# Kernel optimization log

Hardware: AMD Instinct MI355X
Metric: run time of the kernel (lower is better)

The kernel has to match this reference:

```python
import math
import jax, jax.numpy as jnp
import numpy as np

B, T, C, H = 2, 2048, 1024, 16

def setup_inputs() -> dict:
    key = jax.random.key(0)
    k1, k2, k3 = jax.random.split(key, 3)
    x = jax.random.normal(k1, (B, T, C), dtype=jnp.float32)
    W_kqv = jax.random.normal(k2, (C, 3 * C), dtype=jnp.float32) * (1.0 / math.sqrt(C))
    W_proj = jax.random.normal(k3, (C, C), dtype=jnp.float32) * (1.0 / math.sqrt(C))
    b_proj = jnp.zeros((C,), dtype=jnp.float32)
    return {"x": x, "W_kqv": W_kqv, "W_proj": W_proj, "b_proj": b_proj}

def reference(x, W_kqv, W_proj, b_proj):
    Bx, Tx, Cx = x.shape
    hs = Cx // H  # head size
    q, k, v = jnp.split(x @ W_kqv, 3, axis=2)  # each (B,T,C)
    # (B,T,C) -> (B,H,T,hs)
    q = q.reshape(Bx, Tx, H, hs).transpose(0, 2, 1, 3)
    k = k.reshape(Bx, Tx, H, hs).transpose(0, 2, 1, 3)
    v = v.reshape(Bx, Tx, H, hs).transpose(0, 2, 1, 3)
    attn = jnp.einsum('bhqd,bhkd->bhqk', q, k) / math.sqrt(hs)  # (B,H,T,T)
    causal = jnp.tril(jnp.ones((Tx, Tx), dtype=bool))
    attn = jnp.where(causal, attn, -jnp.inf)
    attn = jax.nn.softmax(attn, axis=-1)
    y = jnp.einsum('bhqk,bhkd->bhqd', attn, v)  # (B,H,T,hs)
    y = y.transpose(0, 2, 1, 3).reshape(Bx, Tx, Cx)
    return y @ W_proj + b_proj
```

## Files before the change

### kernel.cpp

```cpp
#include <hip/hip_runtime.h>


typedef unsigned short u16;
typedef unsigned int u32;
typedef __bf16 bf16x8 __attribute__((ext_vector_type(8)));
typedef float f32x4 __attribute__((ext_vector_type(4)));
typedef u32 u32x4 __attribute__((ext_vector_type(4)));
typedef u32 u32x2 __attribute__((ext_vector_type(2)));
typedef u16 u16x4 __attribute__((ext_vector_type(4)));

__device__ __forceinline__ u16 f2bf(float f) {
  u32 u = __float_as_uint(f);
  u32 r = u + 0x7FFFu + ((u >> 16) & 1u);
  return (u16)(r >> 16);
}

__device__ __forceinline__ u32 cvt_pk_bf16(float a, float b) {
  u32 r;
  asm("v_cvt_pk_bf16_f32 %0, %1, %2" : "=v"(r) : "v"(a), "v"(b));
  return r;
}

__device__ __forceinline__ bf16x8 ld_bf8(const u16* p) {
  union { u32x4 u; bf16x8 b; } x;
  x.u = *(const u32x4*)p;
  return x.b;
}

__device__ __forceinline__ void gld_lds16(const u16* g, u16* l) {
  __builtin_amdgcn_global_load_lds(
      (const __attribute__((address_space(1))) u32*)g,
      (__attribute__((address_space(3))) u32*)l, 16, 0, 0);
}

__device__ __forceinline__ void convT_body(const float* __restrict__ src,
                                           u16* __restrict__ dst, int R, int Cc,
                                           int r0, int c0, float* ls ) {
  int t = threadIdx.x;
  for (int u = t; u < 1024; u += 256) {
    int r = u >> 4, cs = (u & 15) << 2;
    float4 v = *(const float4*)&src[(size_t)(r0 + r) * Cc + (c0 + cs)];
    ls[r * 65 + cs] = v.x; ls[r * 65 + cs + 1] = v.y;
    ls[r * 65 + cs + 2] = v.z; ls[r * 65 + cs + 3] = v.w;
  }
  __syncthreads();
  for (int u = t; u < 1024; u += 256) {
    int n = u >> 4, ks = (u & 15) << 2;
    u16x4 o;
    o.x = f2bf(ls[ks * 65 + n]); o.y = f2bf(ls[(ks + 1) * 65 + n]);
    o.z = f2bf(ls[(ks + 2) * 65 + n]); o.w = f2bf(ls[(ks + 3) * 65 + n]);
    *(u16x4*)&dst[(size_t)(c0 + n) * R + (r0 + ks)] = o;
  }
}

__global__ __launch_bounds__(256) void prep_kernel(
    const float* __restrict__ x, const float* __restrict__ Wkqv,
    const float* __restrict__ Wproj, u16* __restrict__ xb,
    u16* __restrict__ wkqvT, u16* __restrict__ wprojT) {
  __shared__ float ls[64 * 65];
  int bx = blockIdx.x;
  if (bx < 2048) {
    int idx = bx * 256 + threadIdx.x;
    const float4* s4 = (const float4*)x;
    float4 a = s4[2 * idx], b = s4[2 * idx + 1];
    union { u16 h[8]; u32x4 v; } pk;
    pk.h[0] = f2bf(a.x); pk.h[1] = f2bf(a.y); pk.h[2] = f2bf(a.z); pk.h[3] = f2bf(a.w);
    pk.h[4] = f2bf(b.x); pk.h[5] = f2bf(b.y); pk.h[6] = f2bf(b.z); pk.h[7] = f2bf(b.w);
    *(u32x4*)&xb[(size_t)idx * 8] = pk.v;
  } else if (bx < 2816) {
    int idx = bx - 2048;
    convT_body(Wkqv, wkqvT, 1024, 3072, (idx & 15) * 64, (idx >> 4) * 64, ls);
  } else {
    int idx = bx - 2816;
    convT_body(Wproj, wprojT, 1024, 1024, (idx & 15) * 64, (idx >> 4) * 64, ls);
  }
}

__global__ __launch_bounds__(256) void qkv_gemm_kernel(
    const u16* __restrict__ A, const u16* __restrict__ Bt,
    u16* __restrict__ Qh, u16* __restrict__ Kh, u16* __restrict__ Vh, float qscale) {
  constexpr int K = 1024;
  __shared__ __align__(16) u16 As[128 * 32];
  __shared__ __align__(16) u16 Bs[128 * 32];
  int t = threadIdx.x;
  int wave = t >> 6, lane = t & 63, quad = lane >> 4, l16 = lane & 15;
  int wm = (wave >> 1) << 6, wn = (wave & 1) << 6;
  int m0 = blockIdx.x * 128, n0 = blockIdx.y * 128;
  f32x4 acc[4][4] = {};
  int u0 = t, u1 = t + 256;
  int ra0 = u0 >> 2, ca0 = ((u0 & 3) ^ ((u0 >> 3) & 3)) << 3;
  int ra1 = u1 >> 2, ca1 = ((u1 & 3) ^ ((u1 >> 3) & 3)) << 3;
  int swq = (quad ^ ((l16 >> 1) & 3)) << 3;
  for (int k0 = 0; k0 < K; k0 += 32) {
    gld_lds16(&A[(size_t)(m0 + ra0) * K + k0 + ca0], &As[u0 * 8]);
    gld_lds16(&A[(size_t)(m0 + ra1) * K + k0 + ca1], &As[u1 * 8]);
    gld_lds16(&Bt[(size_t)(n0 + ra0) * K + k0 + ca0], &Bs[u0 * 8]);
    gld_lds16(&Bt[(size_t)(n0 + ra1) * K + k0 + ca1], &Bs[u1 * 8]);
    __syncthreads();
    bf16x8 af[4], bfr[4];
    for (int r = 0; r < 4; ++r) af[r] = ld_bf8(&As[(wm + r * 16 + l16) * 32 + swq]);
    for (int c = 0; c < 4; ++c) bfr[c] = ld_bf8(&Bs[(wn + c * 16 + l16) * 32 + swq]);
    for (int r = 0; r < 4; ++r)
      for (int c = 0; c < 4; ++c)
        acc[r][c] = __builtin_amdgcn_mfma_f32_16x16x32_bf16(af[r], bfr[c], acc[r][c], 0, 0, 0);
    __syncthreads();
  }
  for (int r = 0; r < 4; ++r) {
    int rowbase = m0 + wm + r * 16 + quad * 4;
    for (int c = 0; c < 4; ++c) {
      int col = n0 + wn + c * 16 + l16;
      int seg = col >> 10;
      int cc = col & 1023;
      int h = cc >> 6, d = cc & 63;
      for (int i = 0; i < 4; ++i) {
        int row = rowbase + i;
        int b = row >> 11, tt = row & 2047;
        size_t off = (((size_t)(b * 16 + h)) * 2048 + tt) * 64 + d;
        float v = acc[r][c][i];
        if (seg == 0)      Qh[off] = f2bf(v * qscale);
        else if (seg == 1) Kh[off] = f2bf(v);
        else               Vh[off] = f2bf(v);
      }
    }
  }
}

__global__ __launch_bounds__(256) void vT_kernel(const u16* __restrict__ Vh,
                                                 u16* __restrict__ Vt) {
  __shared__ __align__(16) u16 ls[64 * 72];
  int t = threadIdx.x;
  int t0 = blockIdx.x * 64, bh = blockIdx.y;
  const u16* in = Vh + ((size_t)bh * 2048 + t0) * 64;
  for (int u = t; u < 512; u += 256) {
    int row = u >> 3, col = (u & 7) << 3;
    *(u32x4*)&ls[row * 72 + col] = *(const u32x4*)&in[(size_t)row * 64 + col];
  }
  __syncthreads();
  for (int u = t; u < 512; u += 256) {
    int d = u >> 3, tc = (u & 7) << 3;
    union { u16 h[8]; u32x4 v; } pk;
    for (int j = 0; j < 8; ++j) pk.h[j] = ls[(tc + j) * 72 + d];
    *(u32x4*)&Vt[((size_t)bh * 64 + d) * 2048 + t0 + tc] = pk.v;
  }
}

__global__ __launch_bounds__(256) void proj_gemm_kernel(
    const u16* __restrict__ A, const u16* __restrict__ Bt,
    float* __restrict__ out, const float* __restrict__ bias) {
  constexpr int K = 1024;
  __shared__ __align__(16) u16 As[64 * 32];
  __shared__ __align__(16) u16 Bs[64 * 32];
  int t = threadIdx.x;
  int wave = t >> 6, lane = t & 63, quad = lane >> 4, l16 = lane & 15;
  int wm = (wave >> 1) << 5, wn = (wave & 1) << 5;
  int m0 = blockIdx.x * 64, n0 = blockIdx.y * 64;
  f32x4 acc[2][2] = {};
  int u0 = t;
  int ra0 = u0 >> 2, ca0 = ((u0 & 3) ^ ((u0 >> 3) & 3)) << 3;
  int swq = (quad ^ ((l16 >> 1) & 3)) << 3;
  for (int k0 = 0; k0 < K; k0 += 32) {
    gld_lds16(&A[(size_t)(m0 + ra0) * K + k0 + ca0], &As[u0 * 8]);
    gld_lds16(&Bt[(size_t)(n0 + ra0) * K + k0 + ca0], &Bs[u0 * 8]);
    __syncthreads();
    bf16x8 af[2], bfr[2];
    for (int r = 0; r < 2; ++r) af[r] = ld_bf8(&As[(wm + r * 16 + l16) * 32 + swq]);
    for (int c = 0; c < 2; ++c) bfr[c] = ld_bf8(&Bs[(wn + c * 16 + l16) * 32 + swq]);
    for (int r = 0; r < 2; ++r)
      for (int c = 0; c < 2; ++c)
        acc[r][c] = __builtin_amdgcn_mfma_f32_16x16x32_bf16(af[r], bfr[c], acc[r][c], 0, 0, 0);
    __syncthreads();
  }
  for (int r = 0; r < 2; ++r) {
    int rowbase = m0 + wm + r * 16 + quad * 4;
    for (int c = 0; c < 2; ++c) {
      int col = n0 + wn + c * 16 + l16;
      float bv = bias[col];
      for (int i = 0; i < 4; ++i)
        out[(size_t)(rowbase + i) * 1024 + col] = acc[r][c][i] + bv;
    }
  }
}

__global__ __launch_bounds__(256, 4) void flash_kernel(
    const u16* __restrict__ Qh, const u16* __restrict__ Kh, const u16* __restrict__ Vt,
    u16* __restrict__ yb, float* __restrict__ Opart) {
  __shared__ __align__(16) u16 Ks[2][64 * 64];
  __shared__ __align__(16) u16 Vs[2][64 * 64];
  int t = threadIdx.x, wave = t >> 6, lane = t & 63, quad = lane >> 4, l16 = lane & 15;
  const unsigned char JT[22] = {9, 8, 7, 47, 63, 46, 62, 6, 45, 61, 44, 60,
                                5, 43, 59, 42, 58, 4, 3, 2, 1, 0};
  int id = blockIdx.x;
  int g = id / 176, r = id % 176;
  int bh = g * 8 + (r & 7);
  int jx = r >> 3;
  int code = JT[jx];
  int qtile = code & 15;
  int half = (code >> 4) & 1;
  bool partial = (code >> 5) != 0;
  int nkv = 2 * qtile + 2, mid = qtile + 1;
  int kvs = (partial && half) ? mid : 0;
  int kve = partial ? (half ? nkv : mid) : nkv;
  int sidx = 15 - qtile;
  int q0 = qtile << 7;
  const u16* Qb = Qh + (size_t)bh * 2048 * 64;
  const u16* Kb = Kh + (size_t)bh * 2048 * 64;
  const u16* Vb = Vt + (size_t)bh * 64 * 2048;
  int qlo = q0 + wave * 32;
  int qhi = qlo + 31;
  bf16x8 qa0, qa1, qa2, qa3;
  {
    int qr0 = qlo + l16;
    qa0 = ld_bf8(&Qb[(size_t)qr0 * 64 + quad * 8]);
    qa1 = ld_bf8(&Qb[(size_t)qr0 * 64 + 32 + quad * 8]);
    int qr1 = qr0 + 16;
    qa2 = ld_bf8(&Qb[(size_t)qr1 * 64 + quad * 8]);
    qa3 = ld_bf8(&Qb[(size_t)qr1 * 64 + 32 + quad * 8]);
  }
  f32x4 oacc0[4] = {}, oacc1[4] = {};
  float lsum0 = 0.f, lsum1 = 0.f;
  int u0 = wave * 128 + lane, u1 = u0 + 64;
  int r0 = u0 >> 3, p0 = u0 & 7, cb0 = (p0 - r0) & 7;
  int r1s = u1 >> 3, p1 = u1 & 7, cb1 = (p1 - r1s) & 7;
  int vsub = (quad & 1) * 4;
  int vc0 = quad >> 1;
  {
    int kv0 = kvs << 6;
    gld_lds16(&Kb[(size_t)(kv0 + r0) * 64 + cb0 * 8], &Ks[0][u0 * 8]);
    gld_lds16(&Kb[(size_t)(kv0 + r1s) * 64 + cb1 * 8], &Ks[0][u1 * 8]);
    gld_lds16(&Vb[(size_t)r0 * 2048 + kv0 + cb0 * 8], &Vs[0][u0 * 8]);
    gld_lds16(&Vb[(size_t)r1s * 2048 + kv0 + cb1 * 8], &Vs[0][u1 * 8]);
  }
  for (int j = kvs; j < kve; ++j) {
    int p = (j - kvs) & 1;
    asm volatile("s_waitcnt vmcnt(0)" ::: "memory");
    __builtin_amdgcn_s_barrier();
    asm volatile("" ::: "memory");
    if (j + 1 < kve) {
      int kn0 = (j + 1) << 6;
      int pn = p ^ 1;
      gld_lds16(&Kb[(size_t)(kn0 + r0) * 64 + cb0 * 8], &Ks[pn][u0 * 8]);
      gld_lds16(&Kb[(size_t)(kn0 + r1s) * 64 + cb1 * 8], &Ks[pn][u1 * 8]);
      gld_lds16(&Vb[(size_t)r0 * 2048 + kn0 + cb0 * 8], &Vs[pn][u0 * 8]);
      gld_lds16(&Vb[(size_t)r1s * 2048 + kn0 + cb1 * 8], &Vs[pn][u1 * 8]);
    }
    int kv0 = j << 6;
    if (kv0 > qhi) continue;
    const u16* Ksp = Ks[p];
    const u16* Vsp = Vs[p];
    bool maskit = (kv0 + 63 > qlo);
    u32 w0[4][2], w1[4][2];
    for (int c = 0; c < 4; ++c) {
      int krow = c * 16 + l16;
      bf16x8 kb0 = ld_bf8(&Ksp[krow * 64 + ((quad + krow) & 7) * 8]);
      bf16x8 kb1 = ld_bf8(&Ksp[krow * 64 + ((quad + 4 + krow) & 7) * 8]);
      f32x4 z0 = {0.f, 0.f, 0.f, 0.f}, z1 = {0.f, 0.f, 0.f, 0.f};
      z0 = __builtin_amdgcn_mfma_f32_16x16x32_bf16(kb0, qa0, z0, 0, 0, 0);
      z0 = __builtin_amdgcn_mfma_f32_16x16x32_bf16(kb1, qa1, z0, 0, 0, 0);
      z1 = __builtin_amdgcn_mfma_f32_16x16x32_bf16(kb0, qa2, z1, 0, 0, 0);
      z1 = __builtin_amdgcn_mfma_f32_16x16x32_bf16(kb1, qa3, z1, 0, 0, 0);
      float pe0[4], pe1[4];
      if (maskit) {
        int qg0 = qlo + l16, qg1 = qg0 + 16;
        for (int i = 0; i < 4; ++i) {
          int kv = kv0 + c * 16 + quad * 4 + i;
          float a = __builtin_amdgcn_exp2f(z0[i]);
          float b = __builtin_amdgcn_exp2f(z1[i]);
          if (kv > qg0) a = 0.f;
          if (kv > qg1) b = 0.f;
          lsum0 += a; lsum1 += b;
          pe0[i] = a; pe1[i] = b;
        }
      } else {
        for (int i = 0; i < 4; ++i) {
          float a = __builtin_amdgcn_exp2f(z0[i]);
          float b = __builtin_amdgcn_exp2f(z1[i]);
          lsum0 += a; lsum1 += b;
          pe0[i] = a; pe1[i] = b;
        }
      }
      w0[c][0] = cvt_pk_bf16(pe0[0], pe0[1]); w0[c][1] = cvt_pk_bf16(pe0[2], pe0[3]);
      w1[c][0] = cvt_pk_bf16(pe1[0], pe1[1]); w1[c][1] = cvt_pk_bf16(pe1[2], pe1[3]);
    }
    union { u32 uu[4]; bf16x8 b; } pf00, pf01, pf10, pf11;
    pf00.uu[0] = w0[0][0]; pf00.uu[1] = w0[0][1]; pf00.uu[2] = w0[1][0]; pf00.uu[3] = w0[1][1];
    pf01.uu[0] = w0[2][0]; pf01.uu[1] = w0[2][1]; pf01.uu[2] = w0[3][0]; pf01.uu[3] = w0[3][1];
    pf10.uu[0] = w1[0][0]; pf10.uu[1] = w1[0][1]; pf10.uu[2] = w1[1][0]; pf10.uu[3] = w1[1][1];
    pf11.uu[0] = w1[2][0]; pf11.uu[1] = w1[2][1]; pf11.uu[2] = w1[3][0]; pf11.uu[3] = w1[3][1];
    for (int dt = 0; dt < 4; ++dt) {
      int vrow = dt * 16 + l16;
      int rbase = vrow * 64 + vsub;
      union { u32x2 lo2; struct { u32 a, b; }; } h0lo, h0hi, h1lo, h1hi;
      h0lo.lo2 = *(const u32x2*)&Vsp[rbase + (((vc0)     + vrow) & 7) * 8];
      h0hi.lo2 = *(const u32x2*)&Vsp[rbase + (((vc0 + 2) + vrow) & 7) * 8];
      h1lo.lo2 = *(const u32x2*)&Vsp[rbase + (((vc0 + 4) + vrow) & 7) * 8];
      h1hi.lo2 = *(const u32x2*)&Vsp[rbase + (((vc0 + 6) + vrow) & 7) * 8];
      union { u32 uu[4]; bf16x8 b; } va0, va1;
      va0.uu[0] = h0lo.a; va0.uu[1] = h0lo.b; va0.uu[2] = h0hi.a; va0.uu[3] = h0hi.b;
      va1.uu[0] = h1lo.a; va1.uu[1] = h1lo.b; va1.uu[2] = h1hi.a; va1.uu[3] = h1hi.b;
      oacc0[dt] = __builtin_amdgcn_mfma_f32_16x16x32_bf16(va0.b, pf00.b, oacc0[dt], 0, 0, 0);
      oacc0[dt] = __builtin_amdgcn_mfma_f32_16x16x32_bf16(va1.b, pf01.b, oacc0[dt], 0, 0, 0);
      oacc1[dt] = __builtin_amdgcn_mfma_f32_16x16x32_bf16(va0.b, pf10.b, oacc1[dt], 0, 0, 0);
      oacc1[dt] = __builtin_amdgcn_mfma_f32_16x16x32_bf16(va1.b, pf11.b, oacc1[dt], 0, 0, 0);
    }
  }
  lsum0 += __shfl_xor(lsum0, 16);
  lsum0 += __shfl_xor(lsum0, 32);
  lsum1 += __shfl_xor(lsum1, 16);
  lsum1 += __shfl_xor(lsum1, 32);
  if (partial) {
    float* Op = Opart + ((size_t)(bh * 6 + sidx) * 2 + half) * 8320;
    int ql = wave * 32 + l16;
    for (int dt = 0; dt < 4; ++dt)
      *(f32x4*)&Op[ql * 64 + dt * 16 + quad * 4] = oacc0[dt];
    for (int dt = 0; dt < 4; ++dt)
      *(f32x4*)&Op[(ql + 16) * 64 + dt * 16 + quad * 4] = oacc1[dt];
    if (quad == 0) { Op[8192 + ql] = lsum0; Op[8192 + ql + 16] = lsum1; }
  } else {
    int b = bh >> 4, hd = bh & 15;
    float inv0 = 1.0f / lsum0, inv1 = 1.0f / lsum1;
    int qq0 = qlo + l16;
    size_t ro0 = ((size_t)(b * 2048 + qq0)) * 1024 + hd * 64;
    size_t ro1 = ro0 + (size_t)16 * 1024;
    for (int dt = 0; dt < 4; ++dt) {
      u32x2 pr;
      pr.x = cvt_pk_bf16(oacc0[dt][0] * inv0, oacc0[dt][1] * inv0);
      pr.y = cvt_pk_bf16(oacc0[dt][2] * inv0, oacc0[dt][3] * inv0);
      *(u32x2*)&yb[ro0 + dt * 16 + quad * 4] = pr;
      pr.x = cvt_pk_bf16(oacc1[dt][0] * inv1, oacc1[dt][1] * inv1);
      pr.y = cvt_pk_bf16(oacc1[dt][2] * inv1, oacc1[dt][3] * inv1);
      *(u32x2*)&yb[ro1 + dt * 16 + quad * 4] = pr;
    }
  }
}

__global__ __launch_bounds__(256) void combine_kernel(const float* __restrict__ Opart,
                                                      u16* __restrict__ yb) {
  int sidx = blockIdx.x, bh = blockIdx.y, t = threadIdx.x;
  int qtile = 15 - sidx;
  const float* A = Opart + (size_t)(bh * 6 + sidx) * 2 * 8320;
  const float* Bp = A + 8320;
  int q = t >> 1, d0 = (t & 1) << 5;
  float inv = 1.0f / (A[8192 + q] + Bp[8192 + q]);
  int b = bh >> 4, h = bh & 15;
  size_t off = ((size_t)(b * 2048 + (qtile << 7) + q)) * 1024 + h * 64 + d0;
  union { u16 hh[32]; u32x4 v[4]; } pk;
  for (int k = 0; k < 32; ++k)
    pk.hh[k] = f2bf((A[q * 64 + d0 + k] + Bp[q * 64 + d0 + k]) * inv);
  for (int s = 0; s < 4; ++s)
    *(u32x4*)&yb[off + s * 8] = pk.v[s];
}

extern "C" void kernel_launch(void* const* d_in, const int* in_sizes, int n_in,
                              void* d_out, int out_size, void* d_ws, size_t ws_size,
                              hipStream_t stream) {
  const float* x     = (const float*)d_in[0];
  const float* Wkqv  = (const float*)d_in[1];
  const float* Wproj = (const float*)d_in[2];
  const float* bproj = (const float*)d_in[3];
  float* out = (float*)d_out;

  u16* ws     = (u16*)d_ws;
  u16* xb     = ws;
  u16* wkqvT  = xb + (size_t)4096 * 1024;
  u16* wprojT = wkqvT + (size_t)3072 * 1024;
  u16* Qh     = wprojT + (size_t)1024 * 1024;
  u16* Kh     = Qh + (size_t)32 * 2048 * 64;
  u16* Vt     = Kh + (size_t)32 * 2048 * 64;
  u16* yb     = Vt + (size_t)32 * 2048 * 64;
  u16* Vh     = yb;
  float* Opart = (float*)ws;

  const float QSCALE = 0.18033688011112042f;

  prep_kernel<<<3072, 256, 0, stream>>>(x, Wkqv, Wproj, xb, wkqvT, wprojT);
  qkv_gemm_kernel<<<dim3(32, 24), 256, 0, stream>>>(xb, wkqvT, Qh, Kh, Vh, QSCALE);
  vT_kernel<<<dim3(32, 32), 256, 0, stream>>>(Vh, Vt);
  flash_kernel<<<704, 256, 0, stream>>>(Qh, Kh, Vt, yb, Opart);
  combine_kernel<<<dim3(6, 32), 256, 0, stream>>>(Opart, yb);
  proj_gemm_kernel<<<dim3(64, 16), 256, 0, stream>>>(yb, wprojT, out, bproj);
}
```

Baseline: 181.1 us.

## Double-buffer GEMM LDS tiles and fuse V transpose into QKV epilogue

Both GEMM kernels now use two LDS buffers, prefetching the next K-slice while MFMAs consume the current one, with one barrier per iteration instead of two. The QKV GEMM epilogue writes V directly in transposed layout (4 contiguous bf16 per store), which removes the separate vT kernel launch and its extra read/write pass. This doubles LDS use per block and relies on the manual vmcnt/barrier sequence being correct for the async LDS loads.

```diff
diff --git a/kernel.cpp b/kernel.cpp
--- a/kernel.cpp
+++ b/kernel.cpp
@@ -78,10 +78,10 @@
 
 __global__ __launch_bounds__(256) void qkv_gemm_kernel(
     const u16* __restrict__ A, const u16* __restrict__ Bt,
-    u16* __restrict__ Qh, u16* __restrict__ Kh, u16* __restrict__ Vh, float qscale) {
+    u16* __restrict__ Qh, u16* __restrict__ Kh, u16* __restrict__ Vt, float qscale) {
   constexpr int K = 1024;
-  __shared__ __align__(16) u16 As[128 * 32];
-  __shared__ __align__(16) u16 Bs[128 * 32];
+  __shared__ __align__(16) u16 As[2][128 * 32];
+  __shared__ __align__(16) u16 Bs[2][128 * 32];
   int t = threadIdx.x;
   int wave = t >> 6, lane = t & 63, quad = lane >> 4, l16 = lane & 15;
   int wm = (wave >> 1) << 6, wn = (wave & 1) << 6;
@@ -91,56 +91,50 @@
   int ra0 = u0 >> 2, ca0 = ((u0 & 3) ^ ((u0 >> 3) & 3)) << 3;
   int ra1 = u1 >> 2, ca1 = ((u1 & 3) ^ ((u1 >> 3) & 3)) << 3;
   int swq = (quad ^ ((l16 >> 1) & 3)) << 3;
+  gld_lds16(&A[(size_t)(m0 + ra0) * K + ca0], &As[0][u0 * 8]);
+  gld_lds16(&A[(size_t)(m0 + ra1) * K + ca1], &As[0][u1 * 8]);
+  gld_lds16(&Bt[(size_t)(n0 + ra0) * K + ca0], &Bs[0][u0 * 8]);
+  gld_lds16(&Bt[(size_t)(n0 + ra1) * K + ca1], &Bs[0][u1 * 8]);
   for (int k0 = 0; k0 < K; k0 += 32) {
-    gld_lds16(&A[(size_t)(m0 + ra0) * K + k0 + ca0], &As[u0 * 8]);
-    gld_lds16(&A[(size_t)(m0 + ra1) * K + k0 + ca1], &As[u1 * 8]);
-    gld_lds16(&Bt[(size_t)(n0 + ra0) * K + k0 + ca0], &Bs[u0 * 8]);
-    gld_lds16(&Bt[(size_t)(n0 + ra1) * K + k0 + ca1], &Bs[u1 * 8]);
-    __syncthreads();
+    int p = (k0 >> 5) & 1;
+    asm volatile("s_waitcnt vmcnt(0)" ::: "memory");
+    __builtin_amdgcn_s_barrier();
+    asm volatile("" ::: "memory");
+    if (k0 + 32 < K) {
+      int kn = k0 + 32, pn = p ^ 1;
+      gld_lds16(&A[(size_t)(m0 + ra0) * K + kn + ca0], &As[pn][u0 * 8]);
+      gld_lds16(&A[(size_t)(m0 + ra1) * K + kn + ca1], &As[pn][u1 * 8]);
+      gld_lds16(&Bt[(size_t)(n0 + ra0) * K + kn + ca0], &Bs[pn][u0 * 8]);
+      gld_lds16(&Bt[(size_t)(n0 + ra1) * K + kn + ca1], &Bs[pn][u1 * 8]);
+    }
     bf16x8 af[4], bfr[4];
-    for (int r = 0; r < 4; ++r) af[r] = ld_bf8(&As[(wm + r * 16 + l16) * 32 + swq]);
-    for (int c = 0; c < 4; ++c) bfr[c] = ld_bf8(&Bs[(wn + c * 16 + l16) * 32 + swq]);
+    for (int r = 0; r < 4; ++r) af[r] = ld_bf8(&As[p][(wm + r * 16 + l16) * 32 + swq]);
+    for (int c = 0; c < 4; ++c) bfr[c] = ld_bf8(&Bs[p][(wn + c * 16 + l16) * 32 + swq]);
     for (int r = 0; r < 4; ++r)
       for (int c = 0; c < 4; ++c)
         acc[r][c] = __builtin_amdgcn_mfma_f32_16x16x32_bf16(af[r], bfr[c], acc[r][c], 0, 0, 0);
-    __syncthreads();
   }
   for (int r = 0; r < 4; ++r) {
     int rowbase = m0 + wm + r * 16 + quad * 4;
+    int b = rowbase >> 11, tt = rowbase & 2047;
     for (int c = 0; c < 4; ++c) {
       int col = n0 + wn + c * 16 + l16;
       int seg = col >> 10;
       int cc = col & 1023;
       int h = cc >> 6, d = cc & 63;
-      for (int i = 0; i < 4; ++i) {
-        int row = rowbase + i;
-        int b = row >> 11, tt = row & 2047;
+      if (seg == 2) {
+        union { u16 hh[4]; u16x4 v; } o;
+        for (int i = 0; i < 4; ++i) o.hh[i] = f2bf(acc[r][c][i]);
+        *(u16x4*)&Vt[((size_t)(b * 16 + h) * 64 + d) * 2048 + tt] = o.v;
+      } else {
         size_t off = (((size_t)(b * 16 + h)) * 2048 + tt) * 64 + d;
-        float v = acc[r][c][i];
-        if (seg == 0)      Qh[off] = f2bf(v * qscale);
-        else if (seg == 1) Kh[off] = f2bf(v);
-        else               Vh[off] = f2bf(v);
+        if (seg == 0) {
+          for (int i = 0; i < 4; ++i) Qh[off + (size_t)i * 64] = f2bf(acc[r][c][i] * qscale);
+        } else {
+          for (int i = 0; i < 4; ++i) Kh[off + (size_t)i * 64] = f2bf(acc[r][c][i]);
+        }
       }
     }
-  }
-}
-
-__global__ __launch_bounds__(256) void vT_kernel(const u16* __restrict__ Vh,
-                                                 u16* __restrict__ Vt) {
-  __shared__ __align__(16) u16 ls[64 * 72];
-  int t = threadIdx.x;
-  int t0 = blockIdx.x * 64, bh = blockIdx.y;
-  const u16* in = Vh + ((size_t)bh * 2048 + t0) * 64;
-  for (int u = t; u < 512; u += 256) {
-    int row = u >> 3, col = (u & 7) << 3;
-    *(u32x4*)&ls[row * 72 + col] = *(const u32x4*)&in[(size_t)row * 64 + col];
-  }
-  __syncthreads();
-  for (int u = t; u < 512; u += 256) {
-    int d = u >> 3, tc = (u & 7) << 3;
-    union { u16 h[8]; u32x4 v; } pk;
-    for (int j = 0; j < 8; ++j) pk.h[j] = ls[(tc + j) * 72 + d];
-    *(u32x4*)&Vt[((size_t)bh * 64 + d) * 2048 + t0 + tc] = pk.v;
   }
 }
 
@@ -148,8 +142,8 @@
     const u16* __restrict__ A, const u16* __restrict__ Bt,
     float* __restrict__ out, const float* __restrict__ bias) {
   constexpr int K = 1024;
-  __shared__ __align__(16) u16 As[64 * 32];
-  __shared__ __align__(16) u16 Bs[64 * 32];
+  __shared__ __align__(16) u16 As[2][64 * 32];
+  __shared__ __align__(16) u16 Bs[2][64 * 32];
   int t = threadIdx.x;
   int wave = t >> 6, lane = t & 63, quad = lane >> 4, l16 = lane & 15;
   int wm = (wave >> 1) << 5, wn = (wave & 1) << 5;
@@ -158,17 +152,24 @@
   int u0 = t;
   int ra0 = u0 >> 2, ca0 = ((u0 & 3) ^ ((u0 >> 3) & 3)) << 3;
   int swq = (quad ^ ((l16 >> 1) & 3)) << 3;
+  gld_lds16(&A[(size_t)(m0 + ra0) * K + ca0], &As[0][u0 * 8]);
+  gld_lds16(&Bt[(size_t)(n0 + ra0) * K + ca0], &Bs[0][u0 * 8]);
   for (int k0 = 0; k0 < K; k0 += 32) {
-    gld_lds16(&A[(size_t)(m0 + ra0) * K + k0 + ca0], &As[u0 * 8]);
-    gld_lds16(&Bt[(size_t)(n0 + ra0) * K + k0 + ca0], &Bs[u0 * 8]);
-    __syncthreads();
+    int p = (k0 >> 5) & 1;
+    asm volatile("s_waitcnt vmcnt(0)" ::: "memory");
+    __builtin_amdgcn_s_barrier();
+    asm volatile("" ::: "memory");
+    if (k0 + 32 < K) {
+      int kn = k0 + 32, pn = p ^ 1;
+      gld_lds16(&A[(size_t)(m0 + ra0) * K + kn + ca0], &As[pn][u0 * 8]);
+      gld_lds16(&Bt[(size_t)(n0 + ra0) * K + kn + ca0], &Bs[pn][u0 * 8]);
+    }
     bf16x8 af[2], bfr[2];
-    for (int r = 0; r < 2; ++r) af[r] = ld_bf8(&As[(wm + r * 16 + l16) * 32 + swq]);
-    for (int c = 0; c < 2; ++c) bfr[c] = ld_bf8(&Bs[(wn + c * 16 + l16) * 32 + swq]);
+    for (int r = 0; r < 2; ++r) af[r] = ld_bf8(&As[p][(wm + r * 16 + l16) * 32 + swq]);
+    for (int c = 0; c < 2; ++c) bfr[c] = ld_bf8(&Bs[p][(wn + c * 16 + l16) * 32 + swq]);
     for (int r = 0; r < 2; ++r)
       for (int c = 0; c < 2; ++c)
         acc[r][c] = __builtin_amdgcn_mfma_f32_16x16x32_bf16(af[r], bfr[c], acc[r][c], 0, 0, 0);
-    __syncthreads();
   }
   for (int r = 0; r < 2; ++r) {
     int rowbase = m0 + wm + r * 16 + quad * 4;
@@ -367,14 +368,12 @@
   u16* Kh     = Qh + (size_t)32 * 2048 * 64;
   u16* Vt     = Kh + (size_t)32 * 2048 * 64;
   u16* yb     = Vt + (size_t)32 * 2048 * 64;
-  u16* Vh     = yb;
   float* Opart = (float*)ws;
 
   const float QSCALE = 0.18033688011112042f;
 
   prep_kernel<<<3072, 256, 0, stream>>>(x, Wkqv, Wproj, xb, wkqvT, wprojT);
-  qkv_gemm_kernel<<<dim3(32, 24), 256, 0, stream>>>(xb, wkqvT, Qh, Kh, Vh, QSCALE);
-  vT_kernel<<<dim3(32, 32), 256, 0, stream>>>(Vh, Vt);
+  qkv_gemm_kernel<<<dim3(32, 24), 256, 0, stream>>>(xb, wkqvT, Qh, Kh, Vt, QSCALE);
   flash_kernel<<<704, 256, 0, stream>>>(Qh, Kh, Vt, yb, Opart);
   combine_kernel<<<dim3(6, 32), 256, 0, stream>>>(Opart, yb);
   proj_gemm_kernel<<<dim3(64, 16), 256, 0, stream>>>(yb, wprojT, out, bproj);
```

After: 194.4 us. 1.07x slower.
